# Kernel optimization log

Measured on AMD Instinct MI355X. Metric: run time of the kernel, lower is better.

## Reference

```python
import jax, jax.numpy as jnp
import numpy as np

NUM_SAMPLES = 5      # samples per line (line_matcher_cfg)
MIN_DIST_PTS = 8.0   # min pixel spacing between samples
TOP_K = 10           # top-k candidate lines for NW matching
GRID_SIZE = 4        # desc map stride
GAP = 0.1            # NW gap penalty


def sample_line_points(line_seg):
    # line_seg: (N, 2, 2) ij endpoints -> pts (N, S, 2), valid (N, S)
    start, end = line_seg[:, 0], line_seg[:, 1]
    lengths = jnp.linalg.norm(end - start, axis=1)
    nsamp = jnp.clip(jnp.floor(lengths / MIN_DIST_PTS), 2.0, float(NUM_SAMPLES))
    k = jnp.arange(NUM_SAMPLES, dtype=line_seg.dtype)
    interval = (end - start) / (nsamp - 1.0)[:, None]          # (N, 2)
    pts = start[:, None, :] + k[None, :, None] * interval[:, None, :]
    valid = k[None, :] < nsamp[:, None]
    pts = jnp.where(valid[..., None], pts, 0.0)                # torch pads with 0
    return pts, valid


def sample_descriptors(desc, pts):
    # Faithful F.grid_sample(bilinear, zeros padding, align_corners=False) after
    # kornia normalize_pixel_coordinates ((size-1) normalization), then L2-norm.
    # desc: (1, D, H, W); pts: (P, 2) ij coords in full-res image.
    D, H, W = desc.shape[1], desc.shape[2], desc.shape[3]
    img_h, img_w = H * GRID_SIZE, W * GRID_SIZE
    xn = 2.0 * pts[:, 1] / (img_w - 1) - 1.0
    yn = 2.0 * pts[:, 0] / (img_h - 1) - 1.0
    ix = ((xn + 1.0) * W - 1.0) / 2.0   # align_corners=False unnormalize
    iy = ((yn + 1.0) * H - 1.0) / 2.0
    x0f = jnp.floor(ix); y0f = jnp.floor(iy)
    wx = ix - x0f; wy = iy - y0f
    x0 = x0f.astype(jnp.int32); y0 = y0f.astype(jnp.int32)
    img = desc[0]

    def gather(xi, yi):
        inb = ((xi >= 0) & (xi < W) & (yi >= 0) & (yi < H)).astype(img.dtype)
        xc = jnp.clip(xi, 0, W - 1); yc = jnp.clip(yi, 0, H - 1)
        return img[:, yc, xc] * inb[None, :]   # (D, P), zeros outside

    v = (gather(x0, y0) * ((1 - wx) * (1 - wy))[None]
         + gather(x0 + 1, y0) * (wx * (1 - wy))[None]
         + gather(x0, y0 + 1) * ((1 - wx) * wy)[None]
         + gather(x0 + 1, y0 + 1) * (wx * wy)[None])
    return v / jnp.linalg.norm(v, axis=0, keepdims=True)


def needleman_wunsch(scores):
    # scores: (B, n, m); sequential DP via nested lax.scan (rows, then cols)
    B, n, m = scores.shape
    s = jnp.transpose(scores, (1, 0, 2)) - GAP  # (n, B, m)

    def row_step(prev_row, srow):               # prev_row (B, m+1), srow (B, m)
        diag = prev_row[:, :-1].T                # (m, B)
        up = prev_row[:, 1:].T                   # (m, B)

        def col_step(left, xs):
            d, u, sc = xs
            cur = jnp.maximum(jnp.maximum(left, u), d + sc)
            return cur, cur

        _, cols = jax.lax.scan(col_step, jnp.zeros((B,), s.dtype), (diag, up, srow.T))
        new_row = jnp.concatenate([jnp.zeros((B, 1), s.dtype), cols.T], axis=1)
        return new_row, None

    final, _ = jax.lax.scan(row_step, jnp.zeros((B, m + 1), s.dtype), s)
    return final[:, -1]


def filter_and_match_lines(scores):
    # scores: (N, M, n, n)
    ls1 = scores.max(3); v1 = (ls1 != -1.0).astype(scores.dtype)
    ls1 = (ls1 * v1).sum(2) / v1.sum(2)
    ls2 = scores.max(2); v2 = (ls2 != -1.0).astype(scores.dtype)
    ls2 = (ls2 * v2).sum(2) / v2.sum(2)
    line_scores = (ls1 + ls2) / 2.0
    topk_lines = jnp.argsort(line_scores, axis=1)[:, -TOP_K:]          # (N, k)
    top = jnp.take_along_axis(scores, topk_lines[:, :, None, None], axis=1)
    top = jnp.concatenate([top, jnp.flip(top, axis=-1)], axis=1)       # (N, 2k, n, n)
    N, top2k, n, m = top.shape
    nw = needleman_wunsch(top.reshape(N * top2k, n, m)).reshape(N, top2k)
    matches = jnp.argmax(nw, axis=1) % (top2k // 2)
    matches = topk_lines[jnp.arange(N), matches]
    return matches, nw


def match_forward(line_seg1, line_seg2, desc1, desc2):
    N, M = line_seg1.shape[0], line_seg2.shape[0]
    pts1, val1 = sample_line_points(line_seg1)
    pts2, val2 = sample_line_points(line_seg2)
    d1 = sample_descriptors(desc1, pts1.reshape(-1, 2))   # (D, N*S)
    d2 = sample_descriptors(desc2, pts2.reshape(-1, 2))   # (D, M*S)
    scores = d1.T @ d2                                    # (N*S, M*S)
    scores = jnp.where(val1.reshape(-1)[:, None], scores, -1.0)
    scores = jnp.where(val2.reshape(-1)[None, :], scores, -1.0)
    scores = scores.reshape(N, NUM_SAMPLES, M, NUM_SAMPLES).transpose(0, 2, 1, 3)
    matches, nw = filter_and_match_lines(scores)
    # cross check
    matches2, _ = filter_and_match_lines(scores.transpose(1, 0, 3, 2))
    mutual = matches2[matches] == jnp.arange(N)
    matches = jnp.where(mutual, matches, -1)
    return matches, nw


def setup_inputs():
    key = jax.random.key(0)
    k1, k2, k3, k4 = jax.random.split(key, 4)
    N = M = 1200; D = 128; H = W = 128
    img = float(H * GRID_SIZE - 1)
    line_seg1 = jax.random.uniform(k1, (N, 2, 2), jnp.float32) * img
    line_seg2 = jax.random.uniform(k2, (M, 2, 2), jnp.float32) * img
    desc1 = jax.random.normal(k3, (1, D, H, W), jnp.float32)
    desc2 = jax.random.normal(k4, (1, D, H, W), jnp.float32)
    return {"line_seg1": line_seg1, "line_seg2": line_seg2, "desc1": desc1, "desc2": desc2}


def reference(line_seg1, line_seg2, desc1, desc2):
    return match_forward(line_seg1, line_seg2, desc1, desc2)
```

## Files before the change

### kernel.cpp

```cpp
#include <hip/hip_runtime.h>
#include <hip/hip_bf16.h>


#define NLINES 1200
#define NS 5
#define DD 128
#define HH 128
#define WW 128
#define HW (HH*WW)
#define IMGM1 511.0f
#define GAPC 0.1f
#define NPAD 1216
#define PPAD (NPAD*NS)
#define KEXT 384
#define NCH (KEXT/32)
#define NGRP (PPAD/16)

typedef __attribute__((ext_vector_type(8))) short short8;
typedef __attribute__((ext_vector_type(4))) float f32x4;

__device__ __forceinline__ void async_cp16(const void* g, void* l) {
    __builtin_amdgcn_global_load_lds(
        (const __attribute__((address_space(1))) void*)g,
        (__attribute__((address_space(3))) void*)l, 16, 0, 0);
}

__global__ void transpose_desc(const float* __restrict__ in1, float* __restrict__ out1,
                               const float* __restrict__ in2, float* __restrict__ out2) {
    const float* in = blockIdx.z ? in2 : in1;
    float* out = blockIdx.z ? out2 : out1;
    __shared__ float t[32][132];
    int s0 = blockIdx.x * 128;
    int d0 = blockIdx.y * 32;
    int tid = threadIdx.x;
    #pragma unroll
    for (int pass = 0; pass < 4; ++pass) {
        int idx = pass * 256 + tid;
        int dr = idx >> 5, si = idx & 31;
        float4 v = *(const float4*)&in[(size_t)(d0 + dr) * HW + s0 + 4 * si];
        *(float4*)&t[dr][4 * si] = v;
    }
    __syncthreads();
    #pragma unroll
    for (int pass = 0; pass < 4; ++pass) {
        int idx = pass * 256 + tid;
        int sr = idx >> 3, di = idx & 7;
        float4 v = { t[4 * di][sr], t[4 * di + 1][sr], t[4 * di + 2][sr], t[4 * di + 3][sr] };
        *(float4*)&out[(size_t)(s0 + sr) * DD + d0 + 4 * di] = v;
    }
}

__global__ void samplepack_kernel(const float* __restrict__ lseg1, const float* __restrict__ lseg2,
                                  const float* __restrict__ tdesc1, const float* __restrict__ tdesc2,
                                  const float* __restrict__ desc1, const float* __restrict__ desc2,
                                  short* __restrict__ Aext, short* __restrict__ Bext,
                                  float* __restrict__ val1, float* __restrict__ val2,
                                  int use_t) {
    int side = blockIdx.y;
    const float* lseg = side ? lseg2 : lseg1;
    const float* tdesc = side ? tdesc2 : tdesc1;
    const float* desc = side ? desc2 : desc1;
    short* Ef = side ? Bext : Aext;
    float* valout = side ? val2 : val1;
    int arole = side ? 0 : 1;

    __shared__ float ds[16][129];
    int g = blockIdx.x;
    int t = threadIdx.x;
    int lane = t & 63, w = t >> 6;

    #pragma unroll
    for (int s = 0; s < 4; ++s) {
        int r = w * 4 + s;
        int pt = g * 16 + r;
        int line = pt / NS;
        int k = pt - line * NS;

        float sy = 0.f, sx = 0.f, ey = 0.f, ex = 0.f;
        if (line < NLINES) {
            sy = lseg[line * 4 + 0]; sx = lseg[line * 4 + 1];
            ey = lseg[line * 4 + 2]; ex = lseg[line * 4 + 3];
        }
        float dy = ey - sy, dx = ex - sx;
        float len = sqrtf(dy * dy + dx * dx);
        float ns = floorf(len * 0.125f);
        ns = fminf(fmaxf(ns, 2.0f), 5.0f);
        float kf = (float)k;
        float validf = (kf < ns) ? 1.0f : 0.0f;
        float py = sy + kf * (dy / (ns - 1.0f));
        float px = sx + kf * (dx / (ns - 1.0f));
        if (validf == 0.0f) { py = 0.0f; px = 0.0f; }

        float xn = 2.0f * px / IMGM1 - 1.0f;
        float yn = 2.0f * py / IMGM1 - 1.0f;
        float ix = ((xn + 1.0f) * (float)WW - 1.0f) * 0.5f;
        float iy = ((yn + 1.0f) * (float)HH - 1.0f) * 0.5f;
        float x0f = floorf(ix), y0f = floorf(iy);
        float wx = ix - x0f, wy = iy - y0f;
        int x0 = (int)x0f, y0 = (int)y0f;

        float w00 = (1.0f - wx) * (1.0f - wy);
        float w10 = wx * (1.0f - wy);
        float w01 = (1.0f - wx) * wy;
        float w11 = wx * wy;

        float v0 = 0.0f, v1 = 0.0f;
        int xs[4] = { x0, x0 + 1, x0,     x0 + 1 };
        int ys[4] = { y0, y0,     y0 + 1, y0 + 1 };
        float ws4[4] = { w00, w10, w01, w11 };
        #pragma unroll
        for (int c = 0; c < 4; ++c) {
            int xi = xs[c], yi = ys[c];
            float inb = (xi >= 0 && xi < WW && yi >= 0 && yi < HH) ? 1.0f : 0.0f;
            int xc = min(max(xi, 0), WW - 1);
            int yc = min(max(yi, 0), HH - 1);
            if (use_t) {
                int base = (yc * WW + xc) * DD;
                v0 += tdesc[base + lane] * inb * ws4[c];
                v1 += tdesc[base + 64 + lane] * inb * ws4[c];
            } else {
                int base = yc * WW + xc;
                v0 += desc[lane * HW + base] * inb * ws4[c];
                v1 += desc[(lane + 64) * HW + base] * inb * ws4[c];
            }
        }
        float ss = v0 * v0 + v1 * v1;
        #pragma unroll
        for (int o = 32; o > 0; o >>= 1) ss += __shfl_xor(ss, o);
        if (ss == 0.0f) ss = 1.0f;
        float nrm = sqrtf(ss);
        ds[r][lane] = v0 / nrm;
        ds[r][64 + lane] = v1 / nrm;
        if (lane == 0) valout[pt] = (line < NLINES) ? validf : 0.0f;
    }
    __syncthreads();

    #pragma unroll
    for (int it = 0; it < 3; ++it) {
        int idx = it * 256 + t;
        int c = idx >> 6, l = idx & 63;
        int q = l >> 4, r = l & 15;
        short8 outv;
        #pragma unroll
        for (int jj = 0; jj < 8; ++jj) {
            int kext = c * 32 + q * 8 + jj;
            int term = kext >> 7, k = kext & 127;
            float x = ds[r][k];
            __hip_bfloat16 h = __float2bfloat16(x);
            short v = *(short*)&h;
            bool lo_term = arole ? (term == 1) : (term == 2);
            if (lo_term) {
                float hf = __bfloat162float(h);
                __hip_bfloat16 lw = __float2bfloat16(x - hf);
                v = *(short*)&lw;
            }
            outv[jj] = v;
        }
        *(short8*)&Ef[((size_t)(g * NCH + c) * 64 + l) * 8] = outv;
    }
}

__launch_bounds__(256, 2)
__global__ void score_kernel(const short* __restrict__ Af, const short* __restrict__ Bf,
                             const float* __restrict__ val1, const float* __restrict__ val2,
                             float* __restrict__ lsc, float* __restrict__ lscT) {
    __shared__ union {
        struct { short B[2][5120]; } st;
        struct { float dump[80 * 161]; float red[16][33]; } ep;
    } u;

    const int t = threadIdx.x;
    const int lane = t & 63;
    const int w = t >> 6;
    const int wm = w >> 1;
    const int wn = w & 1;
    const int gA0 = blockIdx.x * 10;
    const int gB0 = blockIdx.y * 10;

    const short* pa[5];
    #pragma unroll
    for (int ti = 0; ti < 5; ++ti)
        pa[ti] = Af + ((size_t)(gA0 + 5 * wm + ti) * NCH * 64 + lane) * 8;

    f32x4 acc[5][5];
    #pragma unroll
    for (int a = 0; a < 5; ++a)
        #pragma unroll
        for (int b = 0; b < 5; ++b)
            acc[a][b] = (f32x4){0.f, 0.f, 0.f, 0.f};

    auto stageB = [&](int c, int b) {
        if (w < 2) {
            #pragma unroll
            for (int p = 0; p < 5; ++p) {
                int gi = w * 5 + p;
                const short* g = Bf + ((size_t)((gB0 + gi) * NCH + c) * 64 + lane) * 8;
                async_cp16(g, &u.st.B[b][gi * 512]);
            }
        }
    };

    short8 ca[5], na[5];
    stageB(0, 0);
    #pragma unroll
    for (int ti = 0; ti < 5; ++ti) ca[ti] = *(const short8*)(pa[ti]);

    #pragma unroll
    for (int c = 0; c < NCH; ++c) {
        __syncthreads();
        if (c + 1 < NCH) {
            stageB(c + 1, (c + 1) & 1);
            #pragma unroll
            for (int ti = 0; ti < 5; ++ti)
                na[ti] = *(const short8*)(pa[ti] + (c + 1) * 512);
        }
        short8 bf_[5];
        #pragma unroll
        for (int tj = 0; tj < 5; ++tj)
            bf_[tj] = *(const short8*)&u.st.B[c & 1][(5 * wn + tj) * 512 + lane * 8];
        #pragma unroll
        for (int ti = 0; ti < 5; ++ti)
            #pragma unroll
            for (int tj = 0; tj < 5; ++tj)
                acc[ti][tj] = __builtin_amdgcn_mfma_f32_16x16x32_bf16(
                    ca[ti], bf_[tj], acc[ti][tj], 0, 0, 0);
        #pragma unroll
        for (int ti = 0; ti < 5; ++ti) ca[ti] = na[ti];
    }

    const int i0l = blockIdx.x * 32;
    const int j0l = blockIdx.y * 32;
    #pragma unroll
    for (int p = 0; p < 2; ++p) {
        __syncthreads();
        if (wm == p) {
            #pragma unroll
            for (int ti = 0; ti < 5; ++ti) {
                #pragma unroll
                for (int reg = 0; reg < 4; ++reg) {
                    int rloc = 16 * ti + (lane >> 4) * 4 + reg;
                    #pragma unroll
                    for (int tj = 0; tj < 5; ++tj) {
                        int col = 80 * wn + 16 * tj + (lane & 15);
                        u.ep.dump[rloc * 161 + col] = acc[ti][tj][reg];
                    }
                }
            }
        }
        __syncthreads();
        #pragma unroll
        for (int e = 0; e < 2; ++e) {
            int q = t * 2 + e;
            int li = q >> 5, lj = q & 31;
            int i = i0l + 16 * p + li;
            int j = j0l + lj;
            float S[5][5];
            #pragma unroll
            for (int a = 0; a < 5; ++a) {
                float va = val1[i * NS + a];
                #pragma unroll
                for (int b = 0; b < 5; ++b) {
                    float vb = val2[j * NS + b];
                    float sc = u.ep.dump[(li * 5 + a) * 161 + (lj * 5 + b)];
                    S[a][b] = (va != 0.0f && vb != 0.0f) ? sc : -1.0f;
                }
            }
            float sum1 = 0.0f, cnt1 = 0.0f;
            #pragma unroll
            for (int a = 0; a < 5; ++a) {
                float r = S[a][0];
                #pragma unroll
                for (int b = 1; b < 5; ++b) r = fmaxf(r, S[a][b]);
                float v = (r != -1.0f) ? 1.0f : 0.0f;
                sum1 += r * v; cnt1 += v;
            }
            float sum2 = 0.0f, cnt2 = 0.0f;
            #pragma unroll
            for (int b = 0; b < 5; ++b) {
                float r = S[0][b];
                #pragma unroll
                for (int a = 1; a < 5; ++a) r = fmaxf(r, S[a][b]);
                float v = (r != -1.0f) ? 1.0f : 0.0f;
                sum2 += r * v; cnt2 += v;
            }
            float res = (sum1 / cnt1 + sum2 / cnt2) * 0.5f;
            u.ep.red[li][lj] = res;
            if (i < NLINES && j < NLINES) lsc[i * NLINES + j] = res;
        }
        __syncthreads();
        #pragma unroll
        for (int e = 0; e < 2; ++e) {
            int q = t + 256 * e;
            int li = q & 15, lj = q >> 4;
            int i = i0l + 16 * p + li;
            int j = j0l + lj;
            if (i < NLINES && j < NLINES) lscT[j * NLINES + i] = u.ep.red[li][lj];
        }
    }
}

__device__ __forceinline__ float nw5(const float* M) {
    float F[6] = {0, 0, 0, 0, 0, 0};
    #pragma unroll
    for (int x = 0; x < 5; ++x) {
        float diag = F[0];
        float left = 0.0f;
        #pragma unroll
        for (int y = 1; y <= 5; ++y) {
            float up = F[y];
            float cur = fmaxf(fmaxf(left, up), diag + (M[x * 5 + y - 1] - GAPC));
            F[y] = cur; left = cur; diag = up;
        }
    }
    return F[5];
}

__global__ void topk_nw_kernel(const float* __restrict__ lsc, const float* __restrict__ lscT,
                               const short* __restrict__ Af, const short* __restrict__ Bf,
                               const float* __restrict__ val1, const float* __restrict__ val2,
                               int* __restrict__ topk1, int* __restrict__ topk2,
                               float* __restrict__ nwout, float* __restrict__ nw2buf) {
    __shared__ short sh_lds[NCH * 512];
    __shared__ float sbuf[10][25];
    __shared__ int jl[10];
    __shared__ float wv[5];
    __shared__ int wi[5];
    int rb = blockIdx.x;
    int dir = (rb >= NLINES) ? 1 : 0;
    int row = rb - dir * NLINES;
    int t = threadIdx.x;
    int w = t >> 6;
    int lane = t & 63;
    int q = lane >> 4, rr = lane & 15;

    const short* shEf = dir ? Bf : Af;
    const short* cdEf = dir ? Af : Bf;
    const float* ls = dir ? (lscT + (size_t)row * NLINES) : (lsc + (size_t)row * NLINES);
    int* topk = dir ? (topk2 + row * 10) : (topk1 + row * 10);

    for (int idx = t; idx < NCH * 64; idx += 320) {
        int c = idx >> 6, l = idx & 63;
        int lq = l >> 4, lr = l & 15;
        int ptS = row * 5 + min(lr, 4);
        const short* gp = shEf + ((size_t)(ptS >> 4) * NCH * 64 + lq * 16 + (ptS & 15)) * 8
                               + (size_t)c * 512;
        *(short8*)&sh_lds[c * 512 + l * 8] = *(const short8*)gp;
    }

    float val[4];
    #pragma unroll
    for (int s = 0; s < 4; ++s) {
        int j = t + 320 * s;
        val[s] = (j < NLINES) ? ls[j] : -1e30f;
    }
    float bv = -1e30f; int bi = -1;
    #pragma unroll
    for (int s = 0; s < 4; ++s) {
        int j = t + 320 * s;
        if (val[s] >= bv) { bv = val[s]; bi = j; }
    }
    for (int sel = 0; sel < 10; ++sel) {
        float rv = bv; int ri = bi;
        #pragma unroll
        for (int o = 32; o > 0; o >>= 1) {
            float ov = __shfl_xor(rv, o);
            int oi = __shfl_xor(ri, o);
            if (ov > rv || (ov == rv && oi > ri)) { rv = ov; ri = oi; }
        }
        if (lane == 0) { wv[w] = rv; wi[w] = ri; }
        __syncthreads();
        float fv = wv[0]; int fi = wi[0];
        #pragma unroll
        for (int qq = 1; qq < 5; ++qq)
            if (wv[qq] > fv || (wv[qq] == fv && wi[qq] > fi)) { fv = wv[qq]; fi = wi[qq]; }
        if (t == 0) { topk[9 - sel] = fi; jl[9 - sel] = fi; }
        if (fi >= 0 && (fi % 320) == t) {
            val[fi / 320] = -1e30f;
            bv = -1e30f; bi = -1;
            #pragma unroll
            for (int s = 0; s < 4; ++s) {
                int j = t + 320 * s;
                if (val[s] >= bv) { bv = val[s]; bi = j; }
            }
        }
        __syncthreads();
    }

    int c1 = jl[2 * w], c2 = jl[2 * w + 1];
    int ptC = (rr < 8) ? (c1 * 5 + min(rr, 4)) : (c2 * 5 + min(rr - 8, 4));
    const short* cp = cdEf + ((size_t)(ptC >> 4) * NCH * 64 + q * 16 + (ptC & 15)) * 8;

    f32x4 acc = (f32x4){0.f, 0.f, 0.f, 0.f};
    #pragma unroll
    for (int c = 0; c < NCH; ++c) {
        short8 sh = *(const short8*)&sh_lds[c * 512 + lane * 8];
        short8 cb = *(const short8*)(cp + c * 512);
        acc = dir ? __builtin_amdgcn_mfma_f32_16x16x32_bf16(cb, sh, acc, 0, 0, 0)
                  : __builtin_amdgcn_mfma_f32_16x16x32_bf16(sh, cb, acc, 0, 0, 0);
    }
    #pragma unroll
    for (int reg = 0; reg < 4; ++reg) {
        int m = q * 4 + reg, n = rr;
        if (!dir) {
            if (m < 5 && n < 5) sbuf[2 * w][m * 5 + n] = acc[reg];
            if (m < 5 && n >= 8 && n < 13) sbuf[2 * w + 1][m * 5 + (n - 8)] = acc[reg];
        } else {
            if (m < 5 && n < 5) sbuf[2 * w][m * 5 + n] = acc[reg];
            if (m >= 8 && m < 13 && n < 5) sbuf[2 * w + 1][(m - 8) * 5 + n] = acc[reg];
        }
    }
    __syncthreads();

    if (t < 20) {
        int r = t >> 1, rev = t & 1;
        int i = dir ? jl[r] : row;
        int j = dir ? row : jl[r];
        float S[25];
        #pragma unroll
        for (int a = 0; a < 5; ++a) {
            float va = val1[i * NS + a];
            #pragma unroll
            for (int b = 0; b < 5; ++b) {
                float vb = val2[j * NS + b];
                S[a * 5 + b] = (va != 0.0f && vb != 0.0f) ? sbuf[r][a * 5 + b] : -1.0f;
            }
        }
        float M[25];
        #pragma unroll
        for (int x = 0; x < 5; ++x)
            #pragma unroll
            for (int y = 0; y < 5; ++y) {
                if (!dir) M[x * 5 + y] = rev ? S[x * 5 + (4 - y)] : S[x * 5 + y];
                else      M[x * 5 + y] = rev ? S[(4 - y) * 5 + x] : S[y * 5 + x];
            }
        float nwv = nw5(M);
        float* o = dir ? nw2buf : nwout;
        o[row * 20 + rev * 10 + r] = nwv;
    }
}

__global__ void argmax_final_kernel(const float* __restrict__ nw1, const float* __restrict__ nw2,
                                    const int* __restrict__ topk1, const int* __restrict__ topk2,
                                    float* __restrict__ out) {
    __shared__ int mpre[NLINES];
    __shared__ int m2[NLINES];
    int t = threadIdx.x;
    for (int qq = t; qq < 2 * NLINES; qq += 1024) {
        int dir = qq / NLINES, row = qq - dir * NLINES;
        const float* nw = (dir ? nw2 : nw1) + row * 20;
        float best = nw[0]; int bi = 0;
        #pragma unroll
        for (int q = 1; q < 20; ++q) {
            float v = nw[q];
            if (v > best) { best = v; bi = q; }
        }
        int m = (dir ? topk2 : topk1)[row * 10 + (bi % 10)];
        if (dir) m2[row] = m; else mpre[row] = m;
    }
    __syncthreads();
    for (int i = t; i < NLINES; i += 1024) {
        int m = mpre[i];
        out[i] = (m2[m] == i) ? (float)m : -1.0f;
    }
}

extern "C" void kernel_launch(void* const* d_in, const int* in_sizes, int n_in,
                              void* d_out, int out_size, void* d_ws, size_t ws_size,
                              hipStream_t stream) {
    const float* lseg1 = (const float*)d_in[0];
    const float* lseg2 = (const float*)d_in[1];
    const float* desc1 = (const float*)d_in[2];
    const float* desc2 = (const float*)d_in[3];
    float* out = (float*)d_out;

    float* wsf = (float*)d_ws;
    size_t off = 0;
    float* val1 = wsf + off;   off += PPAD;
    float* val2 = wsf + off;   off += PPAD;
    float* lsc = wsf + off;    off += (size_t)NLINES * NLINES;
    float* lscT = wsf + off;   off += (size_t)NLINES * NLINES;
    int* topk1 = (int*)(wsf + off); off += NLINES * 10;
    int* topk2 = (int*)(wsf + off); off += NLINES * 10;
    float* nw2buf = wsf + off; off += NLINES * 20;
    short* Aext = (short*)(wsf + off); off += (size_t)PPAD * KEXT / 2;
    short* Bext = (short*)(wsf + off); off += (size_t)PPAD * KEXT / 2;
    float* tdesc1 = wsf + off; off += (size_t)HW * DD;
    float* tdesc2 = wsf + off; off += (size_t)HW * DD;
    size_t need_full = off * sizeof(float);
    int use_t = (ws_size >= need_full) ? 1 : 0;

    if (use_t) {
        transpose_desc<<<dim3(HW / 128, DD / 32, 2), 256, 0, stream>>>(
            desc1, tdesc1, desc2, tdesc2);
    }
    samplepack_kernel<<<dim3(NGRP, 2), 256, 0, stream>>>(
        lseg1, lseg2, tdesc1, tdesc2, desc1, desc2, Aext, Bext, val1, val2, use_t);

    score_kernel<<<dim3(NPAD / 32, NPAD / 32), 256, 0, stream>>>(Aext, Bext, val1, val2,
                                                                 lsc, lscT);

    topk_nw_kernel<<<2 * NLINES, 320, 0, stream>>>(lsc, lscT, Aext, Bext, val1, val2,
                                                   topk1, topk2, out + NLINES, nw2buf);

    argmax_final_kernel<<<1, 1024, 0, stream>>>(out + NLINES, nw2buf, topk1, topk2, out);
}
```

Before: 181.1 us.

## Shrink score epilogue LDS for higher occupancy and use single-wave top-k selection

The score kernel epilogue now stages the accumulator tile in four quarter passes, one per wave, instead of two half passes. This roughly halves the shared-memory footprint, so launch bounds can be raised to four blocks per CU, at the cost of more barriers and register pressure under the tighter bound. The top-k selection in the NW kernel is moved to a single wavefront holding 19 values per lane, which removes the two block-wide barriers per selection round. The trade-off is that the other four waves sit idle during selection and each round does a serial rescan of 19 values.

```diff
diff --git a/kernel.cpp b/kernel.cpp
--- a/kernel.cpp
+++ b/kernel.cpp
@@ -160,13 +160,13 @@
     }
 }
 
-__launch_bounds__(256, 2)
+__launch_bounds__(256, 4)
 __global__ void score_kernel(const short* __restrict__ Af, const short* __restrict__ Bf,
                              const float* __restrict__ val1, const float* __restrict__ val2,
                              float* __restrict__ lsc, float* __restrict__ lscT) {
     __shared__ union {
         struct { short B[2][5120]; } st;
-        struct { float dump[80 * 161]; float red[16][33]; } ep;
+        struct { float dump[80 * 81]; float red[16][17]; } ep;
     } u;
 
     const int t = threadIdx.x;
@@ -230,71 +230,68 @@
 
     const int i0l = blockIdx.x * 32;
     const int j0l = blockIdx.y * 32;
+    const int q2 = lane >> 4, r2 = lane & 15;
     #pragma unroll
     for (int p = 0; p < 2; ++p) {
-        __syncthreads();
-        if (wm == p) {
-            #pragma unroll
-            for (int ti = 0; ti < 5; ++ti) {
+        #pragma unroll
+        for (int pn = 0; pn < 2; ++pn) {
+            __syncthreads();
+            if (wm == p && wn == pn) {
                 #pragma unroll
-                for (int reg = 0; reg < 4; ++reg) {
-                    int rloc = 16 * ti + (lane >> 4) * 4 + reg;
+                for (int ti = 0; ti < 5; ++ti)
                     #pragma unroll
-                    for (int tj = 0; tj < 5; ++tj) {
-                        int col = 80 * wn + 16 * tj + (lane & 15);
-                        u.ep.dump[rloc * 161 + col] = acc[ti][tj][reg];
+                    for (int reg = 0; reg < 4; ++reg) {
+                        int rloc = 16 * ti + q2 * 4 + reg;
+                        #pragma unroll
+                        for (int tj = 0; tj < 5; ++tj)
+                            u.ep.dump[rloc * 81 + 16 * tj + r2] = acc[ti][tj][reg];
+                    }
+            }
+            __syncthreads();
+            {
+                int li = t >> 4, lj = t & 15;
+                int i = i0l + 16 * p + li;
+                int j = j0l + 16 * pn + lj;
+                float S[5][5];
+                #pragma unroll
+                for (int a = 0; a < 5; ++a) {
+                    float va = val1[i * NS + a];
+                    #pragma unroll
+                    for (int b = 0; b < 5; ++b) {
+                        float vb = val2[j * NS + b];
+                        float sc = u.ep.dump[(li * 5 + a) * 81 + (lj * 5 + b)];
+                        S[a][b] = (va != 0.0f && vb != 0.0f) ? sc : -1.0f;
                     }
                 }
-            }
-        }
-        __syncthreads();
-        #pragma unroll
-        for (int e = 0; e < 2; ++e) {
-            int q = t * 2 + e;
-            int li = q >> 5, lj = q & 31;
-            int i = i0l + 16 * p + li;
-            int j = j0l + lj;
-            float S[5][5];
-            #pragma unroll
-            for (int a = 0; a < 5; ++a) {
-                float va = val1[i * NS + a];
+                float sum1 = 0.0f, cnt1 = 0.0f;
+                #pragma unroll
+                for (int a = 0; a < 5; ++a) {
+                    float r = S[a][0];
+                    #pragma unroll
+                    for (int b = 1; b < 5; ++b) r = fmaxf(r, S[a][b]);
+                    float v = (r != -1.0f) ? 1.0f : 0.0f;
+                    sum1 += r * v; cnt1 += v;
+                }
+                float sum2 = 0.0f, cnt2 = 0.0f;
                 #pragma unroll
                 for (int b = 0; b < 5; ++b) {
-                    float vb = val2[j * NS + b];
-                    float sc = u.ep.dump[(li * 5 + a) * 161 + (lj * 5 + b)];
-                    S[a][b] = (va != 0.0f && vb != 0.0f) ? sc : -1.0f;
+                    float r = S[0][b];
+                    #pragma unroll
+                    for (int a = 1; a < 5; ++a) r = fmaxf(r, S[a][b]);
+                    float v = (r != -1.0f) ? 1.0f : 0.0f;
+                    sum2 += r * v; cnt2 += v;
                 }
-            }
-            float sum1 = 0.0f, cnt1 = 0.0f;
-            #pragma unroll
-            for (int a = 0; a < 5; ++a) {
-                float r = S[a][0];
-                #pragma unroll
-                for (int b = 1; b < 5; ++b) r = fmaxf(r, S[a][b]);
-                float v = (r != -1.0f) ? 1.0f : 0.0f;
-                sum1 += r * v; cnt1 += v;
-            }
-            float sum2 = 0.0f, cnt2 = 0.0f;
-            #pragma unroll
-            for (int b = 0; b < 5; ++b) {
-                float r = S[0][b];
-                #pragma unroll
-                for (int a = 1; a < 5; ++a) r = fmaxf(r, S[a][b]);
-                float v = (r != -1.0f) ? 1.0f : 0.0f;
-                sum2 += r * v; cnt2 += v;
-            }
-            float res = (sum1 / cnt1 + sum2 / cnt2) * 0.5f;
-            u.ep.red[li][lj] = res;
-            if (i < NLINES && j < NLINES) lsc[i * NLINES + j] = res;
-        }
-        __syncthreads();
-        #pragma unroll
-        for (int e = 0; e < 2; ++e) {
-            int q = t + 256 * e;
-            int li = q & 15, lj = q >> 4;
-            int i = i0l + 16 * p + li;
-            int j = j0l + lj;
-            if (i < NLINES && j < NLINES) lscT[j * NLINES + i] = u.ep.red[li][lj];
+                float res = (sum1 / cnt1 + sum2 / cnt2) * 0.5f;
+                u.ep.red[li][lj] = res;
+                if (i < NLINES && j < NLINES) lsc[i * NLINES + j] = res;
+            }
+            __syncthreads();
+            {
+                int lj = t >> 4, li = t & 15;
+                int i = i0l + 16 * p + li;
+                int j = j0l + 16 * pn + lj;
+                if (i < NLINES && j < NLINES) lscT[j * NLINES + i] = u.ep.red[li][lj];
+            }
         }
     }
 }
@@ -323,8 +320,6 @@
     __shared__ short sh_lds[NCH * 512];
     __shared__ float sbuf[10][25];
     __shared__ int jl[10];
-    __shared__ float wv[5];
-    __shared__ int wi[5];
     int rb = blockIdx.x;
     int dir = (rb >= NLINES) ? 1 : 0;
     int row = rb - dir * NLINES;
@@ -347,44 +342,31 @@
         *(short8*)&sh_lds[c * 512 + l * 8] = *(const short8*)gp;
     }
 
-    float val[4];
-    #pragma unroll
-    for (int s = 0; s < 4; ++s) {
-        int j = t + 320 * s;
-        val[s] = (j < NLINES) ? ls[j] : -1e30f;
-    }
-    float bv = -1e30f; int bi = -1;
-    #pragma unroll
-    for (int s = 0; s < 4; ++s) {
-        int j = t + 320 * s;
-        if (val[s] >= bv) { bv = val[s]; bi = j; }
-    }
-    for (int sel = 0; sel < 10; ++sel) {
-        float rv = bv; int ri = bi;
-        #pragma unroll
-        for (int o = 32; o > 0; o >>= 1) {
-            float ov = __shfl_xor(rv, o);
-            int oi = __shfl_xor(ri, o);
-            if (ov > rv || (ov == rv && oi > ri)) { rv = ov; ri = oi; }
-        }
-        if (lane == 0) { wv[w] = rv; wi[w] = ri; }
-        __syncthreads();
-        float fv = wv[0]; int fi = wi[0];
-        #pragma unroll
-        for (int qq = 1; qq < 5; ++qq)
-            if (wv[qq] > fv || (wv[qq] == fv && wi[qq] > fi)) { fv = wv[qq]; fi = wi[qq]; }
-        if (t == 0) { topk[9 - sel] = fi; jl[9 - sel] = fi; }
-        if (fi >= 0 && (fi % 320) == t) {
-            val[fi / 320] = -1e30f;
-            bv = -1e30f; bi = -1;
-            #pragma unroll
-            for (int s = 0; s < 4; ++s) {
-                int j = t + 320 * s;
+    if (w == 0) {
+        float val[19];
+        #pragma unroll
+        for (int s = 0; s < 19; ++s) {
+            int j = lane + 64 * s;
+            val[s] = (j < NLINES) ? ls[j] : -1e30f;
+        }
+        for (int sel = 0; sel < 10; ++sel) {
+            float bv = -1e30f; int bi = -1;
+            #pragma unroll
+            for (int s = 0; s < 19; ++s) {
+                int j = lane + 64 * s;
                 if (val[s] >= bv) { bv = val[s]; bi = j; }
             }
-        }
-        __syncthreads();
-    }
+            #pragma unroll
+            for (int o = 32; o > 0; o >>= 1) {
+                float ov = __shfl_xor(bv, o);
+                int oi = __shfl_xor(bi, o);
+                if (ov > bv || (ov == bv && oi > bi)) { bv = ov; bi = oi; }
+            }
+            if (lane == 0) { topk[9 - sel] = bi; jl[9 - sel] = bi; }
+            if ((bi & 63) == lane) val[bi >> 6] = -1e30f;
+        }
+    }
+    __syncthreads();
 
     int c1 = jl[2 * w], c2 = jl[2 * w + 1];
     int ptC = (rr < 8) ? (c1 * 5 + min(rr, 4)) : (c2 * 5 + min(rr - 8, 4));
```

New measurement: 404.5 us. 2.23x slower.
